# Kernel optimization log

Measured on AMD Instinct MI355X. Metric: run time of the kernel, lower is better.

The kernel has to match this reference:

```python
import jax, jax.numpy as jnp
import numpy as np

DN3D = ('NCDHW', 'OIDHW', 'NCDHW')

def conv_t3d(x, w, stride):
    # PyTorch ConvTranspose3d with padding=0: w is (C_in, C_out, k1,k2,k3).
    # Equivalent dilated conv: flip spatial dims, swap in/out channels,
    # lhs_dilation=stride, padding k-1 on each side.
    wf = jnp.flip(w, axis=(2, 3, 4)).transpose(1, 0, 2, 3, 4)  # (O, I, k, k, k)
    pad = [(k - 1, k - 1) for k in w.shape[2:]]
    dn = jax.lax.conv_dimension_numbers(x.shape, wf.shape, DN3D)
    return jax.lax.conv_general_dilated(x, wf, (1, 1, 1), pad,
                                        lhs_dilation=stride, dimension_numbers=dn)

def conv3d(x, w, stride, pad):
    dn = jax.lax.conv_dimension_numbers(x.shape, w.shape, DN3D)
    return jax.lax.conv_general_dilated(x, w, stride, [(pad, pad)] * 3,
                                        dimension_numbers=dn)

def setup_inputs() -> dict:
    key = jax.random.key(0)
    ks = jax.random.split(key, 7)
    out_ch, emb, p = 4, 256, 8
    B, T, D = 2, 8, 4  # batch, 4th spatial dim, coarse grid (input_size//patch_size)
    s = 0.05
    return {
        'x':  jax.random.normal(ks[0], (B, T, out_ch * emb, D, D, D), jnp.float32),
        'w1': jax.random.normal(ks[1], (out_ch * emb, out_ch * 2, p // 2, p // 2, p // 2), jnp.float32) * s,
        'b1': jax.random.normal(ks[2], (out_ch * 2,), jnp.float32) * s,
        'w2': jax.random.normal(ks[3], (out_ch * 2, out_ch * 2, 4, 4, 4), jnp.float32) * s,
        'b2': jax.random.normal(ks[4], (out_ch * 2,), jnp.float32) * s,
        'w3': jax.random.normal(ks[5], (out_ch, out_ch * 2, 4, 4, 4), jnp.float32) * s,
        'b3': jax.random.normal(ks[6], (out_ch,), jnp.float32) * s,
    }

def reference(x, w1, b1, w2, b2, w3, b3):
    # x: (B, D4, C_in, D1, D2, D3). All 4D kernels are size/stride 1 along D4,
    # so fold D4 into the batch and run 3D (de)convs.
    B, T, C, D, _, _ = x.shape
    h = x.reshape(B * T, C, D, D, D)
    bcast = lambda b: b[None, :, None, None, None]
    h = jnp.tanh(conv_t3d(h, w1, (4, 4, 4)) + bcast(b1))   # -> (BT, 8, 16,16,16)
    h = jnp.tanh(conv_t3d(h, w2, (4, 4, 4)) + bcast(b2))   # -> (BT, 8, 64,64,64)
    h = conv3d(h, w3, (2, 2, 2), 1) + bcast(b3)             # -> (BT, 4, 32,32,32)
    out = h.reshape(B, T, *h.shape[1:])                     # (B, D4, C, 32,32,32)
    return jnp.moveaxis(out, 1, -1)                         # (B, C, 32,32,32, D4)
```

## Files before the change

### kernel.cpp

```cpp
#include <hip/hip_runtime.h>
#include <cstdint>

typedef _Float16 f16x8 __attribute__((ext_vector_type(8)));
typedef float f32x4 __attribute__((ext_vector_type(4)));
typedef _Float16 half2_t __attribute__((ext_vector_type(2)));

__device__ __forceinline__ unsigned pkh2(float a, float b) {
  return __builtin_bit_cast(unsigned, __builtin_amdgcn_cvt_pkrtz(a, b));
}
__device__ __forceinline__ float fast_tanh(float x) {
  float e = __builtin_amdgcn_exp2f(x * 2.885390081777927f);
  return 1.0f - 2.0f * __builtin_amdgcn_rcpf(e + 1.0f);
}

#if __has_builtin(__builtin_amdgcn_fdot2)
__device__ __forceinline__ float dot2h(unsigned a, unsigned b, float c) {
  return __builtin_amdgcn_fdot2(__builtin_bit_cast(half2_t, a),
                                __builtin_bit_cast(half2_t, b), c, false);
}
#else
__device__ __forceinline__ float dot2h(unsigned a, unsigned b, float c) {
  float d;
  asm("v_dot2_f32_f16 %0, %1, %2, %3" : "=v"(d) : "v"(a), "v"(b), "v"(c));
  return d;
}
#endif

template <int ITERS>
__global__ __launch_bounds__(256, 2) void k_stage1(const float* __restrict__ x,
                                                   const float* __restrict__ w1,
                                                   const float* __restrict__ w3,
                                                   float* __restrict__ part,
                                                   unsigned* __restrict__ wtab) {
  constexpr int NS = 32 / ITERS;
  constexpr int KSB = (NS == 8) ? 3 : (NS == 4) ? 2 : (NS == 2) ? 1 : 0;
  __shared__ __align__(16) char lds_raw[64 * 65 * 4];
  unsigned short* As = (unsigned short*)lds_raw;
  unsigned short* Bs = (unsigned short*)(lds_raw + 5120);
  float* Cs = (float*)lds_raw;

  const int tid = threadIdx.x;
  if (blockIdx.x == 0) {
    int l = tid << 2;
#pragma unroll
    for (int j = 0; j < 4; ++j) {
      int d = l + j;
      int slot = d & 3, chU = (d >> 2) & 1, kh = (d >> 3) & 3,
          kd = (d >> 5) & 3, cio = d >> 7;
      int co = (chU << 1) + (slot & 1);
      int kwb = (slot >> 1) << 1;
      int base = ((co << 3) + cio) * 64 + (kd << 4) + (kh << 2) + kwb;
      wtab[d] = pkh2(w3[base], w3[base + 1]);
    }
  }

  const int ks = blockIdx.x & (NS - 1);
  const int bt = (blockIdx.x >> KSB) & 15;
  const int co = blockIdx.x >> (KSB + 4);
  const int w = tid >> 6, lane = tid & 63, lm = lane & 15, q = lane >> 4;
  const int rrow = tid & 63, kgr = tid >> 6;

  f32x4 acc[4];
#pragma unroll
  for (int i = 0; i < 4; ++i) acc[i] = (f32x4){0.f, 0.f, 0.f, 0.f};

  const float* gA = x + (bt << 16) + ((size_t)(ks * ITERS * 32) << 6);
  const float* gB = w1 + (co << 6) + (size_t)(ks * ITERS * 32) * 512;

  float va[2][8], vb[2][8];
#define S1_LOAD(buf, it)                            \
  {                                                 \
    const int kb = (it) * 32 + (kgr << 3);          \
    _Pragma("unroll") for (int j = 0; j < 8; ++j) { \
      va[buf][j] = gA[((kb + j) << 6) | rrow];      \
      vb[buf][j] = gB[(kb + j) * 512 + rrow];       \
    }                                               \
  }
  S1_LOAD(0, 0);
#pragma unroll
  for (int it = 0; it < ITERS; ++it) {
    const int cur = it & 1;
    if (it + 1 < ITERS) S1_LOAD(cur ^ 1, it + 1);
    uint4 pa, pb;
    pa.x = pkh2(va[cur][0], va[cur][1]);
    pa.y = pkh2(va[cur][2], va[cur][3]);
    pa.z = pkh2(va[cur][4], va[cur][5]);
    pa.w = pkh2(va[cur][6], va[cur][7]);
    pb.x = pkh2(vb[cur][0], vb[cur][1]);
    pb.y = pkh2(vb[cur][2], vb[cur][3]);
    pb.z = pkh2(vb[cur][4], vb[cur][5]);
    pb.w = pkh2(vb[cur][6], vb[cur][7]);
    *(uint4*)&As[rrow * 40 + (kgr << 3)] = pa;
    *(uint4*)&Bs[rrow * 40 + (kgr << 3)] = pb;
    __syncthreads();
    f16x8 a = *(const f16x8*)&As[((w << 4) + lm) * 40 + (q << 3)];
#pragma unroll
    for (int nf = 0; nf < 4; ++nf) {
      f16x8 b = *(const f16x8*)&Bs[((nf << 4) + lm) * 40 + (q << 3)];
      acc[nf] = __builtin_amdgcn_mfma_f32_16x16x32_f16(a, b, acc[nf], 0, 0, 0);
    }
    __syncthreads();
  }
#undef S1_LOAD
#pragma unroll
  for (int nf = 0; nf < 4; ++nf)
#pragma unroll
    for (int r = 0; r < 4; ++r) {
      int m = (w << 4) + (q << 2) + r;
      int n = (nf << 4) + lm;
      Cs[m * 65 + n] = acc[nf][r];
    }
  __syncthreads();
  float* dst = part + (((size_t)(((ks << 4) + bt) << 3) + co) << 12);
#pragma unroll
  for (int j = 0; j < 4; ++j) {
    int pos = (tid << 2) + (j << 10);
    int z = pos >> 8, y = (pos >> 4) & 15, xx = pos & 15;
    int m = ((z >> 2) << 4) + ((y >> 2) << 2) + (xx >> 2);
    int n = ((z & 3) << 4) + ((y & 3) << 2);
    float4 v;
    v.x = Cs[m * 65 + n + 0];
    v.y = Cs[m * 65 + n + 1];
    v.z = Cs[m * 65 + n + 2];
    v.w = Cs[m * 65 + n + 3];
    *(float4*)&dst[pos] = v;
  }
}

template <int NSPLIT>
__global__ __launch_bounds__(512) void k_stage23(
    const float* __restrict__ part, const float* __restrict__ w2,
    const float* __restrict__ b2, const float* __restrict__ b3,
    const float* __restrict__ b1, const unsigned* __restrict__ wtab,
    float* __restrict__ out) {
  __shared__ __align__(16) unsigned win_d[2][18 * 34 * 12];
  __shared__ __align__(16) unsigned h1p[6 * 280];
  __shared__ __align__(16) unsigned w2p[8 * 320];

  const int tid = threadIdx.x;
  const int bid = blockIdx.x;
  const int tile = bid & 31;
  const int bt = bid >> 5;
  const int tz = tile >> 3, ty = (tile >> 2) & 1, tx = tile & 3;
  const int Z0 = tz << 3, Y0 = ty << 4, X0 = tx << 3;
  const int Qz0 = (Z0 << 1) - 1, Qy0 = (Y0 << 1) - 1, Qx0 = (X0 << 1) - 1;
  const int Uz0 = Qz0 >> 2, Uy0 = Qy0 >> 2, Ux0 = Qx0 >> 2;

  float sv[6][NSPLIT];
  float b1v[6];
  int dsto[6];
  bool inb[6];
#pragma unroll
  for (int k = 0; k < 6; ++k) {
    int l = tid + (k << 9);
    bool vld = l < 2880;
    int ll = vld ? l : 0;
    int ci = ll / 360;
    int sp = ll - ci * 360;
    int ux = sp % 6;
    int t1 = sp / 6;
    int uy = t1 % 10;
    int uz = t1 / 10;
    int gz = Uz0 + uz, gy = Uy0 + uy, gx = Ux0 + ux;
    inb[k] = vld && (unsigned)gz < 16u && (unsigned)gy < 16u &&
             (unsigned)gx < 16u;
    dsto[k] = vld ? (uz * 560 + uy * 56 + (ux << 3) + ci) : -1;
    b1v[k] = 0.f;
    if (inb[k]) {
      b1v[k] = b1[ci];
      const float* p =
          part + (((size_t)(bt << 3) + ci) << 12) + (gz << 8) + (gy << 4) + gx;
#pragma unroll
      for (int sg = 0; sg < NSPLIT; ++sg) sv[k][sg] = p[(size_t)sg << 19];
    }
  }

  for (int l = tid; l < 2048; l += 512) {
    int j = l & 3, kx = (l >> 2) & 3, kzy = (l >> 4) & 15, cio = l >> 8;
    int kpos = (kzy << 2) + kx;
    float w0 = w2[(((j << 1) << 3) + cio) * 64 + kpos];
    float w1v = w2[((((j << 1) + 1) << 3) + cio) * 64 + kpos];
    w2p[cio * 320 + kzy * 20 + (kx << 2) + j] = pkh2(w0, w1v);
  }
  for (int u = tid; u < 1224; u += 512) {
    int wz = u / 68;
    int rem = u - wz * 68;
    int wy = rem >> 1;
    int half = rem & 1;
    int qz = Qz0 + wz, qy = Qy0 + wy;
    if ((unsigned)qz < 64u && (unsigned)qy < 64u) continue;
    uint4 zz;
    zz.x = zz.y = zz.z = zz.w = 0u;
#pragma unroll
    for (int bsel = 0; bsel < 2; ++bsel) {
      unsigned* wrow = win_d[bsel] + (wz * 34 + wy) * 12;
      if (half == 0) {
        *(uint4*)wrow = zz;
      } else {
        *(uint4*)(wrow + 4) = zz;
        wrow[8] = 0u;
      }
    }
  }

#pragma unroll
  for (int k = 0; k < 6; ++k) {
    if (dsto[k] < 0) continue;
    float v = 0.f;
    if (inb[k]) {
      float s = b1v[k];
#pragma unroll
      for (int sg = 0; sg < NSPLIT; ++sg) s += sv[k][sg];
      v = fast_tanh(s);
    }
    ((_Float16*)h1p)[dsto[k]] = (_Float16)v;
  }

  int fu_row[3], fu_h1[3], fu_w2[3], fu_half[3];
  bool fu_act[3];
#pragma unroll
  for (int k = 0; k < 3; ++k) {
    int u = tid + (k << 9);
    bool act = u < 1224;
    int uu = act ? u : 0;
    int wz = uu / 68;
    int rem = uu - wz * 68;
    int wy = rem >> 1, half = rem & 1;
    int qz = Qz0 + wz, qy = Qy0 + wy;
    fu_act[k] = act && (unsigned)qz < 64u && (unsigned)qy < 64u;
    fu_row[k] = (wz * 34 + wy) * 12;
    int kz = qz & 3, ky = qy & 3;
    fu_w2[k] = ((kz << 2) + ky) * 20;
    int uzp = (qz >> 2) - Uz0, uyp = (qy >> 2) - Uy0;
    fu_h1[k] = uzp * 280 + uyp * 28;
    fu_half[k] = half;
  }
  const bool gLo = (Qx0 >= 0), gHi = (Qx0 + 17 < 64);

  __syncthreads();

  float acc[2][4];
#pragma unroll
  for (int a = 0; a < 2; ++a)
#pragma unroll
    for (int i = 0; i < 4; ++i) acc[a][i] = 0.f;

  const int xh = tid & 1, yq = (tid >> 1) & 15, zq = (tid >> 5) & 7;
  const int chS = __builtin_amdgcn_readfirstlane(tid >> 8);

  for (int cio = 0; cio < 8; ++cio) {
    unsigned* wbuf = win_d[cio & 1];
    const float b2c = b2[cio];
#pragma unroll
    for (int k = 0; k < 3; ++k) {
      if (!fu_act[k]) continue;
      unsigned* wrow = wbuf + fu_row[k];
      const unsigned* w2b = w2p + cio * 320 + fu_w2[k];
      uint4 wv[4];
#pragma unroll
      for (int kx = 0; kx < 4; ++kx) wv[kx] = *(const uint4*)(w2b + (kx << 2));
      const unsigned* h1b = h1p + fu_h1[k];
#define DOT8(hc, kx)                                            \
  dot2h((hc).w, wv[kx].w,                                       \
        dot2h((hc).z, wv[kx].z,                                 \
              dot2h((hc).y, wv[kx].y, dot2h((hc).x, wv[kx].x, b2c))))
      if (fu_half[k] == 0) {
        uint4 h0 = *(const uint4*)(h1b);
        uint4 h1c = *(const uint4*)(h1b + 4);
        uint4 h2c = *(const uint4*)(h1b + 8);
        float vals[8];
        vals[0] = gLo ? fast_tanh(DOT8(h0, 3)) : 0.f;
#pragma unroll
        for (int kx = 0; kx < 4; ++kx) vals[1 + kx] = fast_tanh(DOT8(h1c, kx));
#pragma unroll
        for (int kx = 0; kx < 3; ++kx) vals[5 + kx] = fast_tanh(DOT8(h2c, kx));
        uint4 s0;
        s0.x = pkh2(vals[0], vals[1]);
        s0.y = pkh2(vals[2], vals[3]);
        s0.z = pkh2(vals[4], vals[5]);
        s0.w = pkh2(vals[6], vals[7]);
        *(uint4*)wrow = s0;
      } else {
        uint4 h2c = *(const uint4*)(h1b + 8);
        uint4 h3 = *(const uint4*)(h1b + 12);
        uint4 h4 = *(const uint4*)(h1b + 16);
        uint4 h5 = *(const uint4*)(h1b + 20);
        float vals[10];
        vals[0] = fast_tanh(DOT8(h2c, 3));
#pragma unroll
        for (int kx = 0; kx < 4; ++kx) vals[1 + kx] = fast_tanh(DOT8(h3, kx));
#pragma unroll
        for (int kx = 0; kx < 4; ++kx) vals[5 + kx] = fast_tanh(DOT8(h4, kx));
        vals[9] = gHi ? fast_tanh(DOT8(h5, 0)) : 0.f;
        uint4 s1;
        s1.x = pkh2(vals[0], vals[1]);
        s1.y = pkh2(vals[2], vals[3]);
        s1.z = pkh2(vals[4], vals[5]);
        s1.w = pkh2(vals[6], vals[7]);
        *(uint4*)(wrow + 4) = s1;
        wrow[8] = pkh2(vals[8], vals[9]);
      }
#undef DOT8
    }
    __syncthreads();
#pragma unroll
    for (int kd = 0; kd < 4; ++kd) {
      int wz = (zq << 1) + kd;
#pragma unroll
      for (int kh = 0; kh < 4; ++kh) {
        int wy = (yq << 1) + kh;
        const unsigned* rowp = wbuf + (wz * 34 + wy) * 12 + (xh << 2);
        uint4 rv = *(const uint4*)rowp;
        unsigned r4 = rowp[4];
        unsigned r[5] = {rv.x, rv.y, rv.z, rv.w, r4};
        const uint4 wv =
            *(const uint4*)&wtab[((((cio << 4) + (kd << 2) + kh) << 1) + chS)
                                 << 2];
        unsigned wA[2] = {wv.x, wv.y};
        unsigned wB[2] = {wv.z, wv.w};
#pragma unroll
        for (int cc = 0; cc < 2; ++cc) {
#pragma unroll
          for (int i = 0; i < 4; ++i) {
            float a0 = dot2h(r[i], wA[cc], acc[cc][i]);
            acc[cc][i] = dot2h(r[i + 1], wB[cc], a0);
          }
        }
      }
    }
  }
  const int ch = tid >> 8;
  const int b = bt >> 3, t8 = bt & 7;
  const int z = Z0 + zq;
  const int y = Y0 + yq;
#pragma unroll
  for (int cc = 0; cc < 2; ++cc) {
    int c4 = (ch << 1) + cc;
    float bias = b3[c4];
#pragma unroll
    for (int i = 0; i < 4; ++i) {
      int xx = X0 + (xh << 2) + i;
      out[(((((b << 2) + c4) * 32 + z) * 32 + y) * 32 + xx) << 3 | t8] =
          acc[cc][i] + bias;
    }
  }
}

extern "C" void kernel_launch(void* const* d_in, const int* in_sizes, int n_in,
                              void* d_out, int out_size, void* d_ws,
                              size_t ws_size, hipStream_t stream) {
  (void)in_sizes; (void)n_in; (void)out_size;
  const float* x = (const float*)d_in[0];
  const float* w1 = (const float*)d_in[1];
  const float* b1 = (const float*)d_in[2];
  const float* w2 = (const float*)d_in[3];
  const float* b2 = (const float*)d_in[4];
  const float* w3 = (const float*)d_in[5];
  const float* b3 = (const float*)d_in[6];
  float* out = (float*)d_out;
  float* part = (float*)d_ws;

  const size_t plane = (size_t)16 * 8 * 4096;
  int nsplit = 1;
  if (ws_size >= 4 * plane * 4 + 4096)
    nsplit = 4;
  else if (ws_size >= 2 * plane * 4 + 4096)
    nsplit = 2;
  unsigned* wtab = (unsigned*)(part + (size_t)nsplit * plane);

  switch (nsplit) {
    case 4:
      k_stage1<8><<<dim3(512), dim3(256), 0, stream>>>(x, w1, w3, part, wtab);
      k_stage23<4><<<dim3(512), dim3(512), 0, stream>>>(part, w2, b2, b3, b1,
                                                        wtab, out);
      break;
    case 2:
      k_stage1<16><<<dim3(256), dim3(256), 0, stream>>>(x, w1, w3, part, wtab);
      k_stage23<2><<<dim3(512), dim3(512), 0, stream>>>(part, w2, b2, b3, b1,
                                                        wtab, out);
      break;
    default:
      k_stage1<32><<<dim3(128), dim3(256), 0, stream>>>(x, w1, w3, part, wtab);
      k_stage23<1><<<dim3(512), dim3(512), 0, stream>>>(part, w2, b2, b3, b1,
                                                        wtab, out);
      break;
  }
}
```

Before: 143.3 us.

## Double stage-2/3 block to 1024 threads, one output channel per thread

Stage-2/3 blocks now use 1024 threads instead of 512. Each thread accumulates a single output channel (4 accumulators) rather than two, and the staging loops for h1, w2 packing and window fill are re-strided to match. This raises per-block parallelism and lowers register pressure per thread. In exchange, the shared window reads are duplicated across the two channel halves, and 1024-thread blocks with large LDS use may limit how many blocks fit per CU.

```diff
diff --git a/kernel.cpp b/kernel.cpp
--- a/kernel.cpp
+++ b/kernel.cpp
@@ -128,7 +128,7 @@
 }
 
 template <int NSPLIT>
-__global__ __launch_bounds__(512) void k_stage23(
+__global__ __launch_bounds__(1024) void k_stage23(
     const float* __restrict__ part, const float* __restrict__ w2,
     const float* __restrict__ b2, const float* __restrict__ b3,
     const float* __restrict__ b1, const unsigned* __restrict__ wtab,
@@ -146,13 +146,13 @@
   const int Qz0 = (Z0 << 1) - 1, Qy0 = (Y0 << 1) - 1, Qx0 = (X0 << 1) - 1;
   const int Uz0 = Qz0 >> 2, Uy0 = Qy0 >> 2, Ux0 = Qx0 >> 2;
 
-  float sv[6][NSPLIT];
-  float b1v[6];
-  int dsto[6];
-  bool inb[6];
-#pragma unroll
-  for (int k = 0; k < 6; ++k) {
-    int l = tid + (k << 9);
+  float sv[3][NSPLIT];
+  float b1v[3];
+  int dsto[3];
+  bool inb[3];
+#pragma unroll
+  for (int k = 0; k < 3; ++k) {
+    int l = tid + (k << 10);
     bool vld = l < 2880;
     int ll = vld ? l : 0;
     int ci = ll / 360;
@@ -175,14 +175,14 @@
     }
   }
 
-  for (int l = tid; l < 2048; l += 512) {
+  for (int l = tid; l < 2048; l += 1024) {
     int j = l & 3, kx = (l >> 2) & 3, kzy = (l >> 4) & 15, cio = l >> 8;
     int kpos = (kzy << 2) + kx;
     float w0 = w2[(((j << 1) << 3) + cio) * 64 + kpos];
     float w1v = w2[((((j << 1) + 1) << 3) + cio) * 64 + kpos];
     w2p[cio * 320 + kzy * 20 + (kx << 2) + j] = pkh2(w0, w1v);
   }
-  for (int u = tid; u < 1224; u += 512) {
+  for (int u = tid; u < 1224; u += 1024) {
     int wz = u / 68;
     int rem = u - wz * 68;
     int wy = rem >> 1;
@@ -204,7 +204,7 @@
   }
 
 #pragma unroll
-  for (int k = 0; k < 6; ++k) {
+  for (int k = 0; k < 3; ++k) {
     if (dsto[k] < 0) continue;
     float v = 0.f;
     if (inb[k]) {
@@ -216,11 +216,11 @@
     ((_Float16*)h1p)[dsto[k]] = (_Float16)v;
   }
 
-  int fu_row[3], fu_h1[3], fu_w2[3], fu_half[3];
-  bool fu_act[3];
-#pragma unroll
-  for (int k = 0; k < 3; ++k) {
-    int u = tid + (k << 9);
+  int fu_row[2], fu_h1[2], fu_w2[2], fu_half[2];
+  bool fu_act[2];
+#pragma unroll
+  for (int k = 0; k < 2; ++k) {
+    int u = tid + (k << 10);
     bool act = u < 1224;
     int uu = act ? u : 0;
     int wz = uu / 68;
@@ -239,20 +239,19 @@
 
   __syncthreads();
 
-  float acc[2][4];
-#pragma unroll
-  for (int a = 0; a < 2; ++a)
-#pragma unroll
-    for (int i = 0; i < 4; ++i) acc[a][i] = 0.f;
+  float acc[4];
+#pragma unroll
+  for (int i = 0; i < 4; ++i) acc[i] = 0.f;
 
   const int xh = tid & 1, yq = (tid >> 1) & 15, zq = (tid >> 5) & 7;
   const int chS = __builtin_amdgcn_readfirstlane(tid >> 8);
+  const int chU = chS >> 1, sel = chS & 1;
 
   for (int cio = 0; cio < 8; ++cio) {
     unsigned* wbuf = win_d[cio & 1];
     const float b2c = b2[cio];
 #pragma unroll
-    for (int k = 0; k < 3; ++k) {
+    for (int k = 0; k < 2; ++k) {
       if (!fu_act[k]) continue;
       unsigned* wrow = wbuf + fu_row[k];
       const unsigned* w2b = w2p + cio * 320 + fu_w2[k];
@@ -314,35 +313,27 @@
         unsigned r4 = rowp[4];
         unsigned r[5] = {rv.x, rv.y, rv.z, rv.w, r4};
         const uint4 wv =
-            *(const uint4*)&wtab[((((cio << 4) + (kd << 2) + kh) << 1) + chS)
+            *(const uint4*)&wtab[((((cio << 4) + (kd << 2) + kh) << 1) | chU)
                                  << 2];
-        unsigned wA[2] = {wv.x, wv.y};
-        unsigned wB[2] = {wv.z, wv.w};
-#pragma unroll
-        for (int cc = 0; cc < 2; ++cc) {
-#pragma unroll
-          for (int i = 0; i < 4; ++i) {
-            float a0 = dot2h(r[i], wA[cc], acc[cc][i]);
-            acc[cc][i] = dot2h(r[i + 1], wB[cc], a0);
-          }
+        unsigned wA = sel ? wv.y : wv.x;
+        unsigned wB = sel ? wv.w : wv.z;
+#pragma unroll
+        for (int i = 0; i < 4; ++i) {
+          float a0 = dot2h(r[i], wA, acc[i]);
+          acc[i] = dot2h(r[i + 1], wB, a0);
         }
       }
     }
   }
-  const int ch = tid >> 8;
   const int b = bt >> 3, t8 = bt & 7;
   const int z = Z0 + zq;
   const int y = Y0 + yq;
-#pragma unroll
-  for (int cc = 0; cc < 2; ++cc) {
-    int c4 = (ch << 1) + cc;
-    float bias = b3[c4];
-#pragma unroll
-    for (int i = 0; i < 4; ++i) {
-      int xx = X0 + (xh << 2) + i;
-      out[(((((b << 2) + c4) * 32 + z) * 32 + y) * 32 + xx) << 3 | t8] =
-          acc[cc][i] + bias;
-    }
+  const float bias = b3[chS];
+#pragma unroll
+  for (int i = 0; i < 4; ++i) {
+    int xx = X0 + (xh << 2) + i;
+    out[(((((b << 2) + chS) * 32 + z) * 32 + y) * 32 + xx) << 3 | t8] =
+        acc[i] + bias;
   }
 }
 
@@ -371,18 +362,18 @@
   switch (nsplit) {
     case 4:
       k_stage1<8><<<dim3(512), dim3(256), 0, stream>>>(x, w1, w3, part, wtab);
-      k_stage23<4><<<dim3(512), dim3(512), 0, stream>>>(part, w2, b2, b3, b1,
-                                                        wtab, out);
+      k_stage23<4><<<dim3(512), dim3(1024), 0, stream>>>(part, w2, b2, b3, b1,
+                                                         wtab, out);
       break;
     case 2:
       k_stage1<16><<<dim3(256), dim3(256), 0, stream>>>(x, w1, w3, part, wtab);
-      k_stage23<2><<<dim3(512), dim3(512), 0, stream>>>(part, w2, b2, b3, b1,
-                                                        wtab, out);
+      k_stage23<2><<<dim3(512), dim3(1024), 0, stream>>>(part, w2, b2, b3, b1,
+                                                         wtab, out);
       break;
     default:
       k_stage1<32><<<dim3(128), dim3(256), 0, stream>>>(x, w1, w3, part, wtab);
-      k_stage23<1><<<dim3(512), dim3(512), 0, stream>>>(part, w2, b2, b3, b1,
-                                                        wtab, out);
+      k_stage23<1><<<dim3(512), dim3(1024), 0, stream>>>(part, w2, b2, b3, b1,
+                                                         wtab, out);
       break;
   }
 }
```

Measured after the change: 142.3 us. About the same (-0.7%).
